# Optimization experiments

Hardware: AMD Instinct MI355X
Metric: run time of the kernel (lower is better)

Reference implementation:

```python
import jax, jax.numpy as jnp
import numpy as np

B, N, M = 256, 2207, 16          # graphs per batch, nodes per graph, mid_channel
E = 16777216                      # total edges in the batched graph
C1, C2 = 12, 4                    # global_conv1_dim, global_conv2_dim
H1, H2 = 256, 64                  # FC hidden sizes
EPS = 1e-5                        # LayerNorm / BatchNorm eps
BN_SCALE = 1.0 / np.sqrt(1.0 + EPS)  # eval BatchNorm with running_mean=0, running_var=1


def setup_inputs() -> dict:
    ks = jax.random.split(jax.random.key(0), 16)
    def nrm(i, shape, s):
        return jax.random.normal(ks[i], shape, jnp.float32) * s
    return {
        "x": jax.random.normal(ks[0], (B * N, 1), jnp.float32),
        "edge_index": jax.random.randint(ks[1], (2, E), 0, B * N, dtype=jnp.int32),
        "edge_weight": jax.random.uniform(ks[2], (E,), jnp.float32),
        # GraphConv: lin_rel (with bias) on aggregated neighbors + lin_root on self
        "w_root": nrm(3, (1, M), 0.5),
        "w_rel": nrm(4, (1, M), 0.5),
        "b_rel": jnp.full((M,), 0.01, jnp.float32),
        # LayerNorm over (num_nodes, mid_channel)
        "ln_g": jnp.ones((N, M), jnp.float32),
        "ln_b": jnp.zeros((N, M), jnp.float32),
        # 1x1 conv stacks
        "gc1_w": nrm(5, (C1, M), 0.3), "gc1_b": nrm(6, (C1,), 0.1),
        "bn1_g": jnp.ones((C1,), jnp.float32), "bn1_b": jnp.zeros((C1,), jnp.float32),
        "gc2_w": nrm(7, (C2, C1), 0.3), "gc2_b": nrm(8, (C2,), 0.1),
        "bn2_g": jnp.ones((C2,), jnp.float32), "bn2_b": jnp.zeros((C2,), jnp.float32),
        # FC stack (weights stored [in, out])
        "fc_w1": nrm(9, (C2 * N, H1), 0.02), "fc_b1": jnp.full((H1,), 0.01, jnp.float32),
        "fbn1_g": jnp.ones((H1,), jnp.float32), "fbn1_b": jnp.zeros((H1,), jnp.float32),
        "fc_w2": nrm(10, (H1, H2), 0.1), "fc_b2": jnp.full((H2,), 0.01, jnp.float32),
        "fbn2_g": jnp.ones((H2,), jnp.float32), "fbn2_b": jnp.zeros((H2,), jnp.float32),
        "fc1_w": nrm(11, (H2, 1), 0.1), "fc1_b": jnp.full((1,), 0.01, jnp.float32),
    }


def reference(x, edge_index, edge_weight, w_root, w_rel, b_rel, ln_g, ln_b,
              gc1_w, gc1_b, bn1_g, bn1_b, gc2_w, gc2_b, bn2_g, bn2_b,
              fc_w1, fc_b1, fbn1_g, fbn1_b, fc_w2, fc_b2, fbn2_g, fbn2_b,
              fc1_w, fc1_b):
    src, dst = edge_index[0], edge_index[1]
    # GraphConv: gather source features, weight, scatter-add to destinations
    agg = jax.ops.segment_sum(x[src] * edge_weight[:, None], dst, num_segments=B * N)
    h = jax.nn.relu(agg @ w_rel + b_rel + x @ w_root)          # [B*N, M]
    h = h.reshape(B, N, M)
    # LayerNorm over (N, M) per sample (biased variance, as in torch)
    mu = h.mean(axis=(1, 2), keepdims=True)
    var = ((h - mu) ** 2).mean(axis=(1, 2), keepdims=True)
    h = (h - mu) * jax.lax.rsqrt(var + EPS) * ln_g + ln_b
    h = h.transpose(0, 2, 1)                                   # [B, M, N]
    # 1x1 conv -> relu -> eval-BN (rm=0, rv=1)
    y = jax.nn.relu(jnp.einsum('oc,bcn->bon', gc1_w, h) + gc1_b[None, :, None])
    y = y * (BN_SCALE * bn1_g)[None, :, None] + bn1_b[None, :, None]
    y = jax.nn.relu(jnp.einsum('oc,bcn->bon', gc2_w, y) + gc2_b[None, :, None])
    y = y * (BN_SCALE * bn2_g)[None, :, None] + bn2_b[None, :, None]
    z = y.reshape(B, C2 * N)                                   # channel-major flatten, matches torch view
    z = z @ fc_w1 + fc_b1
    z = jax.nn.relu(z * (BN_SCALE * fbn1_g) + fbn1_b)
    z = z @ fc_w2 + fc_b2
    z = jax.nn.relu(z * (BN_SCALE * fbn2_g) + fbn2_b)
    return z @ fc1_w + fc1_b                                   # [B, 1]
```

## Files before the change

### kernel.cpp

```cpp
#include <hip/hip_runtime.h>
#include <hip/hip_bf16.h>

#define BB   256
#define NN   2207
#define MM   16
#define EE   16777216
#define CC1  12
#define CC2  4
#define HH1  256
#define HH2  64
#define KK1  (CC2*NN)
#define LN_EPS 1e-5f
#define BN_SCALE 0.9999950000374997f
#define NBK  256
#define MAGIC 1946067ull
#define EPB  4096
#define TPB  512
#define EPT  (EPB/TPB)
#define NBLK (EE/EPB)

static __device__ __forceinline__ unsigned bucket_of(int d) {
    return (unsigned)(((unsigned long long)(unsigned)d * MAGIC) >> 32);
}

__global__ __launch_bounds__(TPB, 8)
void k_place4(const int* __restrict__ src, const int* __restrict__ dst,
              const float* __restrict__ ew,
              uint2* __restrict__ recs, unsigned short* __restrict__ stab)
{
    __shared__ unsigned int hist[NBK], start[NBK];
    __shared__ unsigned int wtot[4];

    const int t = threadIdx.x;
    if (t < NBK) hist[t] = 0;
    __syncthreads();

    const int i4base = blockIdx.x * (EPB/4);
    unsigned key[EPT];
    float    wv[EPT];
    unsigned short rk[EPT];
    unsigned char  bk[EPT];
    #pragma unroll
    for (int q = 0; q < EPT/4; ++q) {
        int i4 = i4base + q*TPB + t;
        int4   s4 = reinterpret_cast<const int4*>(src)[i4];
        int4   d4 = reinterpret_cast<const int4*>(dst)[i4];
        float4 w4 = reinterpret_cast<const float4*>(ew)[i4];
        unsigned b0 = bucket_of(d4.x), b1 = bucket_of(d4.y);
        unsigned b2 = bucket_of(d4.z), b3 = bucket_of(d4.w);
        unsigned r0 = atomicAdd(&hist[b0], 1u);
        unsigned r1 = atomicAdd(&hist[b1], 1u);
        unsigned r2 = atomicAdd(&hist[b2], 1u);
        unsigned r3 = atomicAdd(&hist[b3], 1u);
        key[q*4+0] = ((unsigned)s4.x << 12) | (unsigned)(d4.x - (int)(b0*NN));
        key[q*4+1] = ((unsigned)s4.y << 12) | (unsigned)(d4.y - (int)(b1*NN));
        key[q*4+2] = ((unsigned)s4.z << 12) | (unsigned)(d4.z - (int)(b2*NN));
        key[q*4+3] = ((unsigned)s4.w << 12) | (unsigned)(d4.w - (int)(b3*NN));
        wv[q*4+0] = w4.x; wv[q*4+1] = w4.y; wv[q*4+2] = w4.z; wv[q*4+3] = w4.w;
        rk[q*4+0] = (unsigned short)r0; rk[q*4+1] = (unsigned short)r1;
        rk[q*4+2] = (unsigned short)r2; rk[q*4+3] = (unsigned short)r3;
        bk[q*4+0] = (unsigned char)b0; bk[q*4+1] = (unsigned char)b1;
        bk[q*4+2] = (unsigned char)b2; bk[q*4+3] = (unsigned char)b3;
    }
    __syncthreads();

    if (t < NBK) {
        unsigned h = hist[t], v = h;
        #pragma unroll
        for (int off = 1; off < 64; off <<= 1) {
            unsigned u = __shfl_up(v, off);
            if ((t & 63) >= off) v += u;
        }
        start[t] = v - h;
        if ((t & 63) == 63) wtot[t >> 6] = v;
    }
    __syncthreads();
    if (t < NBK) {
        const int w = t >> 6;
        unsigned wo = 0;
        if (w > 0) wo += wtot[0];
        if (w > 1) wo += wtot[1];
        if (w > 2) wo += wtot[2];
        start[t] += wo;
        stab[blockIdx.x * NBK + t] = (unsigned short)(start[t]);
    }
    __syncthreads();

    uint2* rb = recs + (size_t)blockIdx.x * EPB;
    #pragma unroll
    for (int e = 0; e < EPT; ++e)
        rb[start[bk[e]] + (unsigned)rk[e]] =
            make_uint2(key[e], __float_as_uint(wv[e]));
}

#define RTPB 256
__global__ __launch_bounds__(RTPB, 8)
void k_replay3(const uint2* __restrict__ recs, const unsigned short* __restrict__ stab,
               const float* __restrict__ x, float* __restrict__ paggr, int rspl)
{
    __shared__ float acc[NN];
    const int t = threadIdx.x;
    const int j = blockIdx.x & (NBK - 1);
    const int r = blockIdx.x >> 8;
    const int kpr = NBLK / rspl;
    for (int n = t; n < NN; n += RTPB) acc[n] = 0.f;
    __syncthreads();

    const int gid = t >> 4, l16 = t & 15;
    const int kb0 = r * kpr;
    for (int kb_i = gid; kb_i < kpr; kb_i += RTPB/16) {
        const int kb = kb0 + kb_i;
        unsigned s0 = stab[(size_t)kb * NBK + j];
        unsigned s1 = (j < NBK-1) ? (unsigned)stab[(size_t)kb * NBK + j + 1]
                                  : (unsigned)EPB;
        const uint2* rp = recs + (size_t)kb * EPB;
        for (unsigned u = s0 + (unsigned)l16; u < s1; u += 16u) {
            uint2 rec = rp[u];
            atomicAdd(&acc[rec.x & 0xFFFu],
                      x[rec.x >> 12] * __uint_as_float(rec.y));
        }
    }
    __syncthreads();
    float* pa = paggr + ((size_t)r * NBK + j) * NN;
    for (int n = t; n < NN; n += RTPB) pa[n] = acc[n];
}

__global__ __launch_bounds__(512)
void k_ln_conv(const float* __restrict__ x, const float* __restrict__ paggr,
              const float* __restrict__ w_root, const float* __restrict__ w_rel,
              const float* __restrict__ b_rel,
              const float* __restrict__ ln_g, const float* __restrict__ ln_b,
              const float* __restrict__ gc1_w, const float* __restrict__ gc1_b,
              const float* __restrict__ bn1_g, const float* __restrict__ bn1_b,
              const float* __restrict__ gc2_w, const float* __restrict__ gc2_b,
              const float* __restrict__ bn2_g, const float* __restrict__ bn2_b,
              float* __restrict__ z, int rspl)
{
    __shared__ float xs[NN], acc[NN];
    __shared__ float gw1[CC1*MM], gb1[CC1], sb1[CC1], tb1[CC1];
    __shared__ float gw2[CC2*CC1], gb2[CC2], sb2[CC2], tb2[CC2];
    __shared__ float redS[8], redQ[8];
    __shared__ float s_mu, s_rs;

    const int b = blockIdx.x, t = threadIdx.x;
    const float* xb = x + b*NN;
    for (int n = t; n < NN; n += 512) {
        xs[n] = xb[n];
        float a = 0.f;
        for (int r = 0; r < rspl; ++r)
            a += paggr[((size_t)r * NBK + b) * NN + n];
        acc[n] = a;
    }
    if (t < CC1*MM) gw1[t] = gc1_w[t];
    if (t >= 192 && t < 192+CC1) { int o = t-192; gb1[o]=gc1_b[o]; sb1[o]=BN_SCALE*bn1_g[o]; tb1[o]=bn1_b[o]; }
    if (t >= 208 && t < 208+CC2*CC1) gw2[t-208] = gc2_w[t-208];
    if (t >= 240 && t < 240+CC2) { int p=t-240; gb2[p]=gc2_b[p]; sb2[p]=BN_SCALE*bn2_g[p]; tb2[p]=bn2_b[p]; }

    float wr[MM], br[MM], wo[MM];
    #pragma unroll
    for (int m = 0; m < MM; ++m) { wr[m]=w_rel[m]; br[m]=b_rel[m]; wo[m]=w_root[m]; }
    __syncthreads();

    float S = 0.f, Q = 0.f;
    for (int n = t; n < NN; n += 512) {
        float a = acc[n], xv = xs[n];
        #pragma unroll
        for (int m = 0; m < MM; ++m) {
            float h = fmaxf(fmaf(a, wr[m], fmaf(xv, wo[m], br[m])), 0.f);
            S += h; Q += h*h;
        }
    }
    #pragma unroll
    for (int off = 32; off; off >>= 1) { S += __shfl_down(S, off); Q += __shfl_down(Q, off); }
    if ((t & 63) == 0) { redS[t>>6] = S; redQ[t>>6] = Q; }
    __syncthreads();
    if (t == 0) {
        float SS = 0.f, QQ = 0.f;
        #pragma unroll
        for (int i = 0; i < 8; ++i) { SS += redS[i]; QQ += redQ[i]; }
        const float inv = 1.f / (float)(NN*MM);
        float mu = SS * inv;
        float var = QQ * inv - mu*mu;
        s_mu = mu; s_rs = rsqrtf(var + LN_EPS);
    }
    __syncthreads();
    const float mu = s_mu, rs = s_rs;

    float* zb = z + (size_t)b * KK1;
    for (int n = t; n < NN; n += 512) {
        float a = acc[n], xv = xs[n];
        float hn[MM];
        const float4* g4  = reinterpret_cast<const float4*>(ln_g + n*MM);
        const float4* be4 = reinterpret_cast<const float4*>(ln_b + n*MM);
        #pragma unroll
        for (int q = 0; q < 4; ++q) {
            float4 g = g4[q], be = be4[q];
            float gg[4]  = {g.x, g.y, g.z, g.w};
            float bb_[4] = {be.x, be.y, be.z, be.w};
            #pragma unroll
            for (int j = 0; j < 4; ++j) {
                int m = q*4 + j;
                float h = fmaxf(fmaf(a, wr[m], fmaf(xv, wo[m], br[m])), 0.f);
                hn[m] = (h - mu) * rs * gg[j] + bb_[j];
            }
        }
        float y1[CC1];
        #pragma unroll
        for (int o = 0; o < CC1; ++o) {
            float a1 = gb1[o];
            #pragma unroll
            for (int m = 0; m < MM; ++m) a1 = fmaf(gw1[o*MM+m], hn[m], a1);
            y1[o] = fmaxf(a1, 0.f) * sb1[o] + tb1[o];
        }
        #pragma unroll
        for (int p = 0; p < CC2; ++p) {
            float a2 = gb2[p];
            #pragma unroll
            for (int o = 0; o < CC1; ++o) a2 = fmaf(gw2[p*CC1+o], y1[o], a2);
            zb[p*NN + n] = fmaxf(a2, 0.f) * sb2[p] + tb2[p];
        }
    }
}

#define GK_CHUNK 288
__global__ __launch_bounds__(256)
void k_fc1_part(const float* __restrict__ z, const float* __restrict__ W1,
                float* __restrict__ out1_part)
{
    __shared__ float zs[64*36];
    __shared__ float ws_[32*68];
    const int bt = blockIdx.x, jt = blockIdx.y, ks = blockIdx.z;
    const int t = threadIdx.x;
    const int tb = t >> 4, tj = t & 15;
    const int k0 = ks * GK_CHUNK;
    const int kend = min(k0 + GK_CHUNK, KK1);
    float acc[4][4] = {};
    const int zrow = t >> 2, zcol = (t & 3) * 8;
    const int wrow = t >> 3, wcol = (t & 7) * 8;

    for (int kc = k0; kc < kend; kc += 32) {
        const float* zsrc = z + (size_t)(bt*64 + zrow)*KK1 + kc + zcol;
        #pragma unroll
        for (int q = 0; q < 2; ++q) {
            int k = kc + zcol + q*4;
            float4 v;
            if (k + 3 < kend) v = *reinterpret_cast<const float4*>(zsrc + q*4);
            else {
                v.x = (k+0 < kend) ? zsrc[q*4+0] : 0.f;
                v.y = (k+1 < kend) ? zsrc[q*4+1] : 0.f;
                v.z = (k+2 < kend) ? zsrc[q*4+2] : 0.f;
                v.w = (k+3 < kend) ? zsrc[q*4+3] : 0.f;
            }
            *reinterpret_cast<float4*>(&zs[zrow*36 + zcol + q*4]) = v;
        }
        {
            int k = kc + wrow;
            const float* wsrc = W1 + (size_t)k*HH1 + jt*64 + wcol;
            #pragma unroll
            for (int q = 0; q < 2; ++q) {
                float4 v;
                if (k < kend) v = *reinterpret_cast<const float4*>(wsrc + q*4);
                else v = float4{0.f,0.f,0.f,0.f};
                *reinterpret_cast<float4*>(&ws_[wrow*68 + wcol + q*4]) = v;
            }
        }
        __syncthreads();
        #pragma unroll
        for (int kk = 0; kk < 32; ++kk) {
            float4 w4 = *reinterpret_cast<const float4*>(&ws_[kk*68 + tj*4]);
            float zv[4], wv[4] = {w4.x, w4.y, w4.z, w4.w};
            #pragma unroll
            for (int ib = 0; ib < 4; ++ib) zv[ib] = zs[(tb*4+ib)*36 + kk];
            #pragma unroll
            for (int ib = 0; ib < 4; ++ib)
                #pragma unroll
                for (int ij = 0; ij < 4; ++ij)
                    acc[ib][ij] = fmaf(zv[ib], wv[ij], acc[ib][ij]);
        }
        __syncthreads();
    }
    #pragma unroll
    for (int ib = 0; ib < 4; ++ib) {
        int row = bt*64 + tb*4 + ib;
        float4 v = make_float4(acc[ib][0], acc[ib][1], acc[ib][2], acc[ib][3]);
        *reinterpret_cast<float4*>(
            &out1_part[((size_t)ks*256 + row)*HH1 + jt*64 + tj*4]) = v;
    }
}

__global__ __launch_bounds__(256)
void k_tail_part(const float* __restrict__ out1_part,
            const float* __restrict__ fc_b1, const float* __restrict__ fbn1_g,
            const float* __restrict__ fbn1_b,
            const float* __restrict__ W2, const float* __restrict__ fc_b2,
            const float* __restrict__ fbn2_g, const float* __restrict__ fbn2_b,
            const float* __restrict__ fc1_w, const float* __restrict__ fc1_b,
            float* __restrict__ out)
{
    __shared__ float o1s[HH1];
    const int b = blockIdx.x, t = threadIdx.x;
    float raw = fc_b1[t];
    #pragma unroll 4
    for (int ks = 0; ks < 31; ++ks)
        raw += out1_part[((size_t)ks*256 + b)*HH1 + t];
    o1s[t] = fmaxf(raw * (BN_SCALE * fbn1_g[t]) + fbn1_b[t], 0.f);
    __syncthreads();
    if (t < HH2) {
        float acc = fc_b2[t];
        #pragma unroll 4
        for (int j = 0; j < HH1; ++j) acc = fmaf(o1s[j], W2[j*HH2 + t], acc);
        float v2 = fmaxf(acc * (BN_SCALE * fbn2_g[t]) + fbn2_b[t], 0.f);
        float c = v2 * fc1_w[t];
        #pragma unroll
        for (int off = 32; off; off >>= 1) c += __shfl_down(c, off);
        if (t == 0) out[b] = c + fc1_b[0];
    }
}

__global__ __launch_bounds__(256)
void k_edge(const int* __restrict__ src, const int* __restrict__ dst,
            const float* __restrict__ ew, const float* __restrict__ x,
            float* __restrict__ agg)
{
    int i = blockIdx.x * 256 + threadIdx.x;
    const int4   s4 = reinterpret_cast<const int4*>(src)[i];
    const int4   d4 = reinterpret_cast<const int4*>(dst)[i];
    const float4 w4 = reinterpret_cast<const float4*>(ew)[i];
    unsafeAtomicAdd(&agg[d4.x], x[s4.x] * w4.x);
    unsafeAtomicAdd(&agg[d4.y], x[s4.y] * w4.y);
    unsafeAtomicAdd(&agg[d4.z], x[s4.z] * w4.z);
    unsafeAtomicAdd(&agg[d4.w], x[s4.w] * w4.w);
}

__global__ __launch_bounds__(256)
void k_sample(const float* __restrict__ x, const float* __restrict__ agg,
              const float* __restrict__ w_root, const float* __restrict__ w_rel,
              const float* __restrict__ b_rel,
              const float* __restrict__ ln_g, const float* __restrict__ ln_b,
              const float* __restrict__ gc1_w, const float* __restrict__ gc1_b,
              const float* __restrict__ bn1_g, const float* __restrict__ bn1_b,
              const float* __restrict__ gc2_w, const float* __restrict__ gc2_b,
              const float* __restrict__ bn2_g, const float* __restrict__ bn2_b,
              float* __restrict__ z)
{
    __shared__ float xs[NN], as[NN];
    __shared__ float gw1[CC1*MM], gb1[CC1], sb1[CC1], tb1[CC1];
    __shared__ float gw2[CC2*CC1], gb2[CC2], sb2[CC2], tb2[CC2];
    __shared__ float redS[4], redQ[4];
    __shared__ float s_mu, s_rs;

    const int b = blockIdx.x, t = threadIdx.x;
    const float* xb = x + b*NN;
    const float* ab = agg + b*NN;
    for (int n = t; n < NN; n += 256) { xs[n] = xb[n]; as[n] = ab[n]; }
    if (t < CC1*MM) gw1[t] = gc1_w[t];
    if (t >= 192 && t < 192+CC1) { int o = t-192; gb1[o]=gc1_b[o]; sb1[o]=BN_SCALE*bn1_g[o]; tb1[o]=bn1_b[o]; }
    if (t >= 208 && t < 208+CC2*CC1) gw2[t-208] = gc2_w[t-208];
    if (t >= 240 && t < 240+CC2) { int p=t-240; gb2[p]=gc2_b[p]; sb2[p]=BN_SCALE*bn2_g[p]; tb2[p]=bn2_b[p]; }

    float wr[MM], br[MM], wo[MM];
    #pragma unroll
    for (int m = 0; m < MM; ++m) { wr[m]=w_rel[m]; br[m]=b_rel[m]; wo[m]=w_root[m]; }
    __syncthreads();

    float S = 0.f, Q = 0.f;
    for (int n = t; n < NN; n += 256) {
        float a = as[n], xv = xs[n];
        #pragma unroll
        for (int m = 0; m < MM; ++m) {
            float h = fmaxf(fmaf(a, wr[m], fmaf(xv, wo[m], br[m])), 0.f);
            S += h; Q += h*h;
        }
    }
    #pragma unroll
    for (int off = 32; off; off >>= 1) { S += __shfl_down(S, off); Q += __shfl_down(Q, off); }
    if ((t & 63) == 0) { redS[t>>6] = S; redQ[t>>6] = Q; }
    __syncthreads();
    if (t == 0) {
        float SS = redS[0]+redS[1]+redS[2]+redS[3];
        float QQ = redQ[0]+redQ[1]+redQ[2]+redQ[3];
        const float inv = 1.f / (float)(NN*MM);
        float mu = SS * inv;
        float var = QQ * inv - mu*mu;
        s_mu = mu; s_rs = rsqrtf(var + LN_EPS);
    }
    __syncthreads();
    const float mu = s_mu, rs = s_rs;

    float* zb = z + (size_t)b * KK1;
    for (int n = t; n < NN; n += 256) {
        float a = as[n], xv = xs[n];
        float hn[MM];
        const float4* g4  = reinterpret_cast<const float4*>(ln_g + n*MM);
        const float4* be4 = reinterpret_cast<const float4*>(ln_b + n*MM);
        #pragma unroll
        for (int q = 0; q < 4; ++q) {
            float4 g = g4[q], be = be4[q];
            float gg[4]  = {g.x, g.y, g.z, g.w};
            float bb_[4] = {be.x, be.y, be.z, be.w};
            #pragma unroll
            for (int j = 0; j < 4; ++j) {
                int m = q*4 + j;
                float h = fmaxf(fmaf(a, wr[m], fmaf(xv, wo[m], br[m])), 0.f);
                hn[m] = (h - mu) * rs * gg[j] + bb_[j];
            }
        }
        float y1[CC1];
        #pragma unroll
        for (int o = 0; o < CC1; ++o) {
            float a1 = gb1[o];
            #pragma unroll
            for (int m = 0; m < MM; ++m) a1 = fmaf(gw1[o*MM+m], hn[m], a1);
            y1[o] = fmaxf(a1, 0.f) * sb1[o] + tb1[o];
        }
        #pragma unroll
        for (int p = 0; p < CC2; ++p) {
            float a2 = gb2[p];
            #pragma unroll
            for (int o = 0; o < CC1; ++o) a2 = fmaf(gw2[p*CC1+o], y1[o], a2);
            zb[p*NN + n] = fmaxf(a2, 0.f) * sb2[p] + tb2[p];
        }
    }
}

__global__ __launch_bounds__(256)
void k_fc1(const float* __restrict__ z, const float* __restrict__ W1,
           float* __restrict__ out1_raw)
{
    __shared__ float zs[64*36];
    __shared__ float ws_[32*68];
    const int bt = blockIdx.x, jt = blockIdx.y, ks = blockIdx.z;
    const int t = threadIdx.x;
    const int tb = t >> 4, tj = t & 15;
    const int k0 = ks * GK_CHUNK;
    const int kend = min(k0 + GK_CHUNK, KK1);
    float acc[4][4] = {};
    const int zrow = t >> 2, zcol = (t & 3) * 8;
    const int wrow = t >> 3, wcol = (t & 7) * 8;

    for (int kc = k0; kc < kend; kc += 32) {
        const float* zsrc = z + (size_t)(bt*64 + zrow)*KK1 + kc + zcol;
        #pragma unroll
        for (int q = 0; q < 2; ++q) {
            int k = kc + zcol + q*4;
            float4 v;
            if (k + 3 < kend) v = *reinterpret_cast<const float4*>(zsrc + q*4);
            else {
                v.x = (k+0 < kend) ? zsrc[q*4+0] : 0.f;
                v.y = (k+1 < kend) ? zsrc[q*4+1] : 0.f;
                v.z = (k+2 < kend) ? zsrc[q*4+2] : 0.f;
                v.w = (k+3 < kend) ? zsrc[q*4+3] : 0.f;
            }
            *reinterpret_cast<float4*>(&zs[zrow*36 + zcol + q*4]) = v;
        }
        {
            int k = kc + wrow;
            const float* wsrc = W1 + (size_t)k*HH1 + jt*64 + wcol;
            #pragma unroll
            for (int q = 0; q < 2; ++q) {
                float4 v;
                if (k < kend) v = *reinterpret_cast<const float4*>(wsrc + q*4);
                else v = float4{0.f,0.f,0.f,0.f};
                *reinterpret_cast<float4*>(&ws_[wrow*68 + wcol + q*4]) = v;
            }
        }
        __syncthreads();
        #pragma unroll
        for (int kk = 0; kk < 32; ++kk) {
            float4 w4 = *reinterpret_cast<const float4*>(&ws_[kk*68 + tj*4]);
            float zv[4], wv[4] = {w4.x, w4.y, w4.z, w4.w};
            #pragma unroll
            for (int ib = 0; ib < 4; ++ib) zv[ib] = zs[(tb*4+ib)*36 + kk];
            #pragma unroll
            for (int ib = 0; ib < 4; ++ib)
                #pragma unroll
                for (int ij = 0; ij < 4; ++ij)
                    acc[ib][ij] = fmaf(zv[ib], wv[ij], acc[ib][ij]);
        }
        __syncthreads();
    }
    #pragma unroll
    for (int ib = 0; ib < 4; ++ib) {
        int row = bt*64 + tb*4 + ib;
        #pragma unroll
        for (int ij = 0; ij < 4; ++ij)
            unsafeAtomicAdd(&out1_raw[row*HH1 + jt*64 + tj*4 + ij], acc[ib][ij]);
    }
}

__global__ __launch_bounds__(256)
void k_tail(const float* __restrict__ out1_raw,
            const float* __restrict__ fc_b1, const float* __restrict__ fbn1_g,
            const float* __restrict__ fbn1_b,
            const float* __restrict__ W2, const float* __restrict__ fc_b2,
            const float* __restrict__ fbn2_g, const float* __restrict__ fbn2_b,
            const float* __restrict__ fc1_w, const float* __restrict__ fc1_b,
            float* __restrict__ out)
{
    __shared__ float o1s[HH1];
    const int b = blockIdx.x, t = threadIdx.x;
    float raw = out1_raw[b*HH1 + t] + fc_b1[t];
    o1s[t] = fmaxf(raw * (BN_SCALE * fbn1_g[t]) + fbn1_b[t], 0.f);
    __syncthreads();
    if (t < HH2) {
        float acc = fc_b2[t];
        #pragma unroll 4
        for (int j = 0; j < HH1; ++j) acc = fmaf(o1s[j], W2[j*HH2 + t], acc);
        float v2 = fmaxf(acc * (BN_SCALE * fbn2_g[t]) + fbn2_b[t], 0.f);
        float c = v2 * fc1_w[t];
        #pragma unroll
        for (int off = 32; off; off >>= 1) c += __shfl_down(c, off);
        if (t == 0) out[b] = c + fc1_b[0];
    }
}

extern "C" void kernel_launch(void* const* d_in, const int* in_sizes, int n_in,
                              void* d_out, int out_size, void* d_ws, size_t ws_size,
                              hipStream_t stream)
{
    const float* x      = (const float*)d_in[0];
    const int*   ei     = (const int*)  d_in[1];
    const float* ew     = (const float*)d_in[2];
    const float* w_root = (const float*)d_in[3];
    const float* w_rel  = (const float*)d_in[4];
    const float* b_rel  = (const float*)d_in[5];
    const float* ln_g   = (const float*)d_in[6];
    const float* ln_b   = (const float*)d_in[7];
    const float* gc1_w  = (const float*)d_in[8];
    const float* gc1_b  = (const float*)d_in[9];
    const float* bn1_g  = (const float*)d_in[10];
    const float* bn1_b  = (const float*)d_in[11];
    const float* gc2_w  = (const float*)d_in[12];
    const float* gc2_b  = (const float*)d_in[13];
    const float* bn2_g  = (const float*)d_in[14];
    const float* bn2_b  = (const float*)d_in[15];
    const float* fc_w1  = (const float*)d_in[16];
    const float* fc_b1  = (const float*)d_in[17];
    const float* fbn1_g = (const float*)d_in[18];
    const float* fbn1_b = (const float*)d_in[19];
    const float* fc_w2  = (const float*)d_in[20];
    const float* fc_b2  = (const float*)d_in[21];
    const float* fbn2_g = (const float*)d_in[22];
    const float* fbn2_b = (const float*)d_in[23];
    const float* fc1_w  = (const float*)d_in[24];
    const float* fc1_b  = (const float*)d_in[25];
    float* out = (float*)d_out;

    char* ws = (char*)d_ws;
    const size_t off_recs  = 0;
    const size_t off_stab  = off_recs + (size_t)NBLK*EPB*8;
    const size_t off_paggr = off_stab + (size_t)NBLK*NBK*2;
    const size_t o1p_sz    = (size_t)31*HH1*256*4;

    int rspl = 8;
    size_t pg_sz   = (size_t)rspl*NBK*NN*4;
    if (pg_sz < o1p_sz) pg_sz = o1p_sz;
    size_t off_zbuf = off_paggr + pg_sz;
    size_t need     = off_zbuf + (size_t)BB*KK1*4;
    if (ws_size < need) {
        rspl = 4;
        pg_sz = (size_t)rspl*NBK*NN*4;
        off_zbuf = off_paggr + pg_sz;
        need = off_zbuf + (size_t)BB*KK1*4;
    }

    if (ws_size >= need) {
        uint2*          recs  = (uint2*)(ws + off_recs);
        unsigned short* stab  = (unsigned short*)(ws + off_stab);
        float*          paggr = (float*)(ws + off_paggr);
        float*          zbuf  = (float*)(ws + off_zbuf);
        float*          o1p   = (float*)(ws + off_paggr);

        k_place4<<<NBLK, TPB, 0, stream>>>(ei, ei + EE, ew, recs, stab);
        k_replay3<<<NBK*rspl, RTPB, 0, stream>>>(recs, stab, x, paggr, rspl);
        k_ln_conv<<<BB, 512, 0, stream>>>(x, paggr,
                                         w_root, w_rel, b_rel, ln_g, ln_b,
                                         gc1_w, gc1_b, bn1_g, bn1_b,
                                         gc2_w, gc2_b, bn2_g, bn2_b, zbuf, rspl);
        k_fc1_part<<<dim3(4,4,31), 256, 0, stream>>>(zbuf, fc_w1, o1p);
        k_tail_part<<<BB, 256, 0, stream>>>(o1p, fc_b1, fbn1_g, fbn1_b,
                                       fc_w2, fc_b2, fbn2_g, fbn2_b,
                                       fc1_w, fc1_b, out);
    } else {
        float* agg      = (float*)(ws);
        float* zbuf     = (float*)(ws + 2259968);
        float* out1_raw = (float*)(ws + 2259968 + 9039872);

        hipMemsetAsync(agg,      0, (size_t)BB*NN*sizeof(float),  stream);
        hipMemsetAsync(out1_raw, 0, (size_t)BB*HH1*sizeof(float), stream);

        k_edge<<<EE/4/256, 256, 0, stream>>>(ei, ei + EE, ew, x, agg);
        k_sample<<<BB, 256, 0, stream>>>(x, agg, w_root, w_rel, b_rel, ln_g, ln_b,
                                         gc1_w, gc1_b, bn1_g, bn1_b,
                                         gc2_w, gc2_b, bn2_g, bn2_b, zbuf);
        k_fc1<<<dim3(4,4,31), 256, 0, stream>>>(zbuf, fc_w1, out1_raw);
        k_tail<<<BB, 256, 0, stream>>>(out1_raw, fc_b1, fbn1_g, fbn1_b,
                                       fc_w2, fc_b2, fbn2_g, fbn2_b,
                                       fc1_w, fc1_b, out);
    }
}
```

Measured before the change: 314.5 us.

## Replace per-block bucket records with global counting sort into contiguous per-graph segments

Edge bucketing becomes a full counting sort: a count pass builds per-block bucket histograms, a scan computes global per-bucket bases, and the placement pass writes each graph's edges into one contiguous padded segment. The replay kernel then streams that segment with 16-byte loads, split into a fixed number of slices, instead of walking thousands of small per-block ranges through a stab table. This is meant to remove the short, uneven inner loops and the stab lookups in replay. The price is an extra full read of dst plus two small scan launches, and the scratch layout is fixed at four slices.

```diff
diff --git a/kernel.cpp b/kernel.cpp
--- a/kernel.cpp
+++ b/kernel.cpp
@@ -18,21 +18,95 @@
 #define TPB  512
 #define EPT  (EPB/TPB)
 #define NBLK (EE/EPB)
+#define RSPL 4
 
 static __device__ __forceinline__ unsigned bucket_of(int d) {
     return (unsigned)(((unsigned long long)(unsigned)d * MAGIC) >> 32);
 }
 
-__global__ __launch_bounds__(TPB, 8)
-void k_place4(const int* __restrict__ src, const int* __restrict__ dst,
-              const float* __restrict__ ew,
-              uint2* __restrict__ recs, unsigned short* __restrict__ stab)
-{
-    __shared__ unsigned int hist[NBK], start[NBK];
-    __shared__ unsigned int wtot[4];
-
+__global__ __launch_bounds__(TPB)
+void k_cnt(const int* __restrict__ dst, unsigned int* __restrict__ cnt)
+{
+    __shared__ unsigned int hist[NBK];
     const int t = threadIdx.x;
     if (t < NBK) hist[t] = 0;
+    __syncthreads();
+    const int i4base = blockIdx.x * (EPB/4);
+    #pragma unroll
+    for (int q = 0; q < EPT/4; ++q) {
+        int4 d4 = reinterpret_cast<const int4*>(dst)[i4base + q*TPB + t];
+        atomicAdd(&hist[bucket_of(d4.x)], 1u);
+        atomicAdd(&hist[bucket_of(d4.y)], 1u);
+        atomicAdd(&hist[bucket_of(d4.z)], 1u);
+        atomicAdd(&hist[bucket_of(d4.w)], 1u);
+    }
+    __syncthreads();
+    if (t < NBK) cnt[blockIdx.x * NBK + t] = hist[t];
+}
+
+__global__ __launch_bounds__(256)
+void k_scan(const unsigned int* __restrict__ cnt,
+            unsigned int* __restrict__ base, unsigned int* __restrict__ lens)
+{
+    __shared__ unsigned int wsum[4];
+    const int j = blockIdx.x, t = threadIdx.x, w = t >> 6;
+    unsigned run = 0;
+    for (int c = 0; c < NBLK/256; ++c) {
+        int blk = c*256 + t;
+        unsigned v = cnt[blk * NBK + j];
+        unsigned s = v;
+        #pragma unroll
+        for (int off = 1; off < 64; off <<= 1) {
+            unsigned u = __shfl_up(s, off);
+            if ((t & 63) >= off) s += u;
+        }
+        if ((t & 63) == 63) wsum[w] = s;
+        __syncthreads();
+        unsigned wo = 0, tot = 0;
+        #pragma unroll
+        for (int k = 0; k < 4; ++k) { unsigned x = wsum[k]; tot += x; if (k < w) wo += x; }
+        base[blk * NBK + j] = run + wo + (s - v);
+        run += tot;
+        __syncthreads();
+    }
+    if (t == 0) lens[j] = run;
+}
+
+__global__ __launch_bounds__(256)
+void k_off(const unsigned int* __restrict__ lens, unsigned int* __restrict__ off,
+           uint2* __restrict__ pairs)
+{
+    __shared__ unsigned int wsum[4];
+    const int t = threadIdx.x, w = t >> 6;
+    unsigned len = lens[t];
+    unsigned pl = (len + 3u) & ~3u;
+    unsigned s = pl;
+    #pragma unroll
+    for (int o = 1; o < 64; o <<= 1) {
+        unsigned u = __shfl_up(s, o);
+        if ((t & 63) >= o) s += u;
+    }
+    if ((t & 63) == 63) wsum[w] = s;
+    __syncthreads();
+    unsigned wo = 0;
+    #pragma unroll
+    for (int k = 0; k < 4; ++k) if (k < w) wo += wsum[k];
+    unsigned o0 = wo + s - pl;
+    off[t] = o0;
+    if (t == 255) off[256] = o0 + pl;
+    for (unsigned g = len; g < pl; ++g) pairs[o0 + g] = make_uint2(0u, 0u);
+}
+
+__global__ __launch_bounds__(TPB, 8)
+void k_place_d(const int* __restrict__ src, const int* __restrict__ dst,
+               const float* __restrict__ ew,
+               const unsigned int* __restrict__ base,
+               const unsigned int* __restrict__ off,
+               uint2* __restrict__ pairs)
+{
+    __shared__ unsigned int hist[NBK], babs[NBK];
+    const int t = threadIdx.x;
+    if (t < NBK) { hist[t] = 0; babs[t] = off[t] + base[blockIdx.x * NBK + t]; }
     __syncthreads();
 
     const int i4base = blockIdx.x * (EPB/4);
@@ -62,67 +136,38 @@
         bk[q*4+0] = (unsigned char)b0; bk[q*4+1] = (unsigned char)b1;
         bk[q*4+2] = (unsigned char)b2; bk[q*4+3] = (unsigned char)b3;
     }
-    __syncthreads();
-
-    if (t < NBK) {
-        unsigned h = hist[t], v = h;
-        #pragma unroll
-        for (int off = 1; off < 64; off <<= 1) {
-            unsigned u = __shfl_up(v, off);
-            if ((t & 63) >= off) v += u;
-        }
-        start[t] = v - h;
-        if ((t & 63) == 63) wtot[t >> 6] = v;
-    }
-    __syncthreads();
-    if (t < NBK) {
-        const int w = t >> 6;
-        unsigned wo = 0;
-        if (w > 0) wo += wtot[0];
-        if (w > 1) wo += wtot[1];
-        if (w > 2) wo += wtot[2];
-        start[t] += wo;
-        stab[blockIdx.x * NBK + t] = (unsigned short)(start[t]);
-    }
-    __syncthreads();
-
-    uint2* rb = recs + (size_t)blockIdx.x * EPB;
     #pragma unroll
     for (int e = 0; e < EPT; ++e)
-        rb[start[bk[e]] + (unsigned)rk[e]] =
+        pairs[(size_t)babs[bk[e]] + (unsigned)rk[e]] =
             make_uint2(key[e], __float_as_uint(wv[e]));
 }
 
-#define RTPB 256
-__global__ __launch_bounds__(RTPB, 8)
-void k_replay3(const uint2* __restrict__ recs, const unsigned short* __restrict__ stab,
-               const float* __restrict__ x, float* __restrict__ paggr, int rspl)
+#define RCB 512
+__global__ __launch_bounds__(RCB, 8)
+void k_replay_c(const uint2* __restrict__ pairs, const unsigned int* __restrict__ off,
+                const float* __restrict__ x, float* __restrict__ paggr)
 {
     __shared__ float acc[NN];
     const int t = threadIdx.x;
     const int j = blockIdx.x & (NBK - 1);
     const int r = blockIdx.x >> 8;
-    const int kpr = NBLK / rspl;
-    for (int n = t; n < NN; n += RTPB) acc[n] = 0.f;
-    __syncthreads();
-
-    const int gid = t >> 4, l16 = t & 15;
-    const int kb0 = r * kpr;
-    for (int kb_i = gid; kb_i < kpr; kb_i += RTPB/16) {
-        const int kb = kb0 + kb_i;
-        unsigned s0 = stab[(size_t)kb * NBK + j];
-        unsigned s1 = (j < NBK-1) ? (unsigned)stab[(size_t)kb * NBK + j + 1]
-                                  : (unsigned)EPB;
-        const uint2* rp = recs + (size_t)kb * EPB;
-        for (unsigned u = s0 + (unsigned)l16; u < s1; u += 16u) {
-            uint2 rec = rp[u];
-            atomicAdd(&acc[rec.x & 0xFFFu],
-                      x[rec.x >> 12] * __uint_as_float(rec.y));
-        }
+    for (int n = t; n < NN; n += RCB) acc[n] = 0.f;
+    __syncthreads();
+
+    const unsigned o0 = off[j], o1 = off[j + 1];
+    const uint4* p4 = reinterpret_cast<const uint4*>(pairs + o0);
+    const unsigned n4 = (o1 - o0) >> 1;
+    const unsigned q = (n4 + RSPL - 1) / RSPL;
+    const unsigned lo = (unsigned)r * q;
+    const unsigned hi = min(lo + q, n4);
+    for (unsigned e = lo + (unsigned)t; e < hi; e += RCB) {
+        uint4 a = p4[e];
+        atomicAdd(&acc[a.x & 0xFFFu], x[a.x >> 12] * __uint_as_float(a.y));
+        atomicAdd(&acc[a.z & 0xFFFu], x[a.z >> 12] * __uint_as_float(a.w));
     }
     __syncthreads();
     float* pa = paggr + ((size_t)r * NBK + j) * NN;
-    for (int n = t; n < NN; n += RTPB) pa[n] = acc[n];
+    for (int n = t; n < NN; n += RCB) pa[n] = acc[n];
 }
 
 __global__ __launch_bounds__(512)
@@ -134,7 +179,7 @@
               const float* __restrict__ bn1_g, const float* __restrict__ bn1_b,
               const float* __restrict__ gc2_w, const float* __restrict__ gc2_b,
               const float* __restrict__ bn2_g, const float* __restrict__ bn2_b,
-              float* __restrict__ z, int rspl)
+              float* __restrict__ z)
 {
     __shared__ float xs[NN], acc[NN];
     __shared__ float gw1[CC1*MM], gb1[CC1], sb1[CC1], tb1[CC1];
@@ -147,7 +192,8 @@
     for (int n = t; n < NN; n += 512) {
         xs[n] = xb[n];
         float a = 0.f;
-        for (int r = 0; r < rspl; ++r)
+        #pragma unroll
+        for (int r = 0; r < RSPL; ++r)
             a += paggr[((size_t)r * NBK + b) * NN + n];
         acc[n] = a;
     }
@@ -547,36 +593,36 @@
     float* out = (float*)d_out;
 
     char* ws = (char*)d_ws;
-    const size_t off_recs  = 0;
-    const size_t off_stab  = off_recs + (size_t)NBLK*EPB*8;
-    const size_t off_paggr = off_stab + (size_t)NBLK*NBK*2;
-    const size_t o1p_sz    = (size_t)31*HH1*256*4;
-
-    int rspl = 8;
-    size_t pg_sz   = (size_t)rspl*NBK*NN*4;
-    if (pg_sz < o1p_sz) pg_sz = o1p_sz;
-    size_t off_zbuf = off_paggr + pg_sz;
-    size_t need     = off_zbuf + (size_t)BB*KK1*4;
-    if (ws_size < need) {
-        rspl = 4;
-        pg_sz = (size_t)rspl*NBK*NN*4;
-        off_zbuf = off_paggr + pg_sz;
-        need = off_zbuf + (size_t)BB*KK1*4;
-    }
+    const size_t off_pairs = 0;
+    const size_t sz_pairs  = (size_t)(EE + 1024) * 8;
+    const size_t off_offs  = off_pairs + sz_pairs;
+    const size_t off_R     = off_offs + 4096;
+    const size_t sz_R      = (size_t)RSPL*NBK*NN*4;
+    const size_t off_cnt   = off_R;
+    const size_t off_base  = off_R + (size_t)NBLK*NBK*4;
+    const size_t off_lens  = off_R + 2*(size_t)NBLK*NBK*4;
+    const size_t off_zbuf  = off_R + sz_R;
+    const size_t need      = off_zbuf + (size_t)BB*KK1*4;
 
     if (ws_size >= need) {
-        uint2*          recs  = (uint2*)(ws + off_recs);
-        unsigned short* stab  = (unsigned short*)(ws + off_stab);
-        float*          paggr = (float*)(ws + off_paggr);
-        float*          zbuf  = (float*)(ws + off_zbuf);
-        float*          o1p   = (float*)(ws + off_paggr);
-
-        k_place4<<<NBLK, TPB, 0, stream>>>(ei, ei + EE, ew, recs, stab);
-        k_replay3<<<NBK*rspl, RTPB, 0, stream>>>(recs, stab, x, paggr, rspl);
+        uint2*        pairs = (uint2*)(ws + off_pairs);
+        unsigned int* offs  = (unsigned int*)(ws + off_offs);
+        unsigned int* cnt   = (unsigned int*)(ws + off_cnt);
+        unsigned int* base  = (unsigned int*)(ws + off_base);
+        unsigned int* lens  = (unsigned int*)(ws + off_lens);
+        float*        paggr = (float*)(ws + off_R);
+        float*        zbuf  = (float*)(ws + off_zbuf);
+        float*        o1p   = (float*)(ws + off_R);
+
+        k_cnt<<<NBLK, TPB, 0, stream>>>(ei + EE, cnt);
+        k_scan<<<NBK, 256, 0, stream>>>(cnt, base, lens);
+        k_off<<<1, 256, 0, stream>>>(lens, offs, pairs);
+        k_place_d<<<NBLK, TPB, 0, stream>>>(ei, ei + EE, ew, base, offs, pairs);
+        k_replay_c<<<NBK*RSPL, RCB, 0, stream>>>(pairs, offs, x, paggr);
         k_ln_conv<<<BB, 512, 0, stream>>>(x, paggr,
                                          w_root, w_rel, b_rel, ln_g, ln_b,
                                          gc1_w, gc1_b, bn1_g, bn1_b,
-                                         gc2_w, gc2_b, bn2_g, bn2_b, zbuf, rspl);
+                                         gc2_w, gc2_b, bn2_g, bn2_b, zbuf);
         k_fc1_part<<<dim3(4,4,31), 256, 0, stream>>>(zbuf, fc_w1, o1p);
         k_tail_part<<<BB, 256, 0, stream>>>(o1p, fc_b1, fbn1_g, fbn1_b,
                                        fc_w2, fc_b2, fbn2_g, fbn2_b,
```

New measurement: 350.6 us. 1.11x slower.

## Replay four buckets per wavefront with prefetched offsets and more region splits

Applied to the files above, without the earlier changes.

The edge-replay kernel now gives each block a group of four adjacent destination buckets, each held in its own LDS accumulator. A full 64-lane wavefront walks the contiguous record span of all four buckets at once, instead of 16 lanes per single bucket. The bucket offsets for the next region are prefetched while the current one is processed, and the work is split into 16 region chunks rather than 8. The aim is better lane utilisation and fewer dependent offset loads, at the cost of twice as many partial aggregates written and summed in the LayerNorm kernel, and more LDS per block.

```diff
diff --git a/kernel.cpp b/kernel.cpp
--- a/kernel.cpp
+++ b/kernel.cpp
@@ -18,6 +18,9 @@
 #define TPB  512
 #define EPT  (EPB/TPB)
 #define NBLK (EE/EPB)
+#define GRP  4
+#define NGRP (NBK/GRP)
+#define RSP6 16
 
 static __device__ __forceinline__ unsigned bucket_of(int d) {
     return (unsigned)(((unsigned long long)(unsigned)d * MAGIC) >> 32);
@@ -93,36 +96,47 @@
             make_uint2(key[e], __float_as_uint(wv[e]));
 }
 
-#define RTPB 256
-__global__ __launch_bounds__(RTPB, 8)
-void k_replay3(const uint2* __restrict__ recs, const unsigned short* __restrict__ stab,
-               const float* __restrict__ x, float* __restrict__ paggr, int rspl)
-{
-    __shared__ float acc[NN];
+__global__ __launch_bounds__(512, 8)
+void k_replay6(const uint2* __restrict__ recs, const unsigned short* __restrict__ stab,
+               const float* __restrict__ x, float* __restrict__ paggr)
+{
+    __shared__ float acc[GRP*NN];
     const int t = threadIdx.x;
-    const int j = blockIdx.x & (NBK - 1);
-    const int r = blockIdx.x >> 8;
-    const int kpr = NBLK / rspl;
-    for (int n = t; n < NN; n += RTPB) acc[n] = 0.f;
-    __syncthreads();
-
-    const int gid = t >> 4, l16 = t & 15;
-    const int kb0 = r * kpr;
-    for (int kb_i = gid; kb_i < kpr; kb_i += RTPB/16) {
-        const int kb = kb0 + kb_i;
-        unsigned s0 = stab[(size_t)kb * NBK + j];
-        unsigned s1 = (j < NBK-1) ? (unsigned)stab[(size_t)kb * NBK + j + 1]
-                                  : (unsigned)EPB;
-        const uint2* rp = recs + (size_t)kb * EPB;
-        for (unsigned u = s0 + (unsigned)l16; u < s1; u += 16u) {
+    const int g = blockIdx.x & (NGRP - 1);
+    const int r = blockIdx.x >> 6;
+    for (int n = t; n < GRP*NN; n += 512) acc[n] = 0.f;
+    __syncthreads();
+
+    const int lane = t & 63, w = t >> 6;
+    const int nreg = NBLK / RSP6;
+    const int reg0 = r * nreg;
+    const int j0 = g * GRP;
+
+    int region = reg0 + w;
+    const unsigned short* sb = stab + (size_t)region * NBK + j0;
+    unsigned c0 = sb[0], c1 = sb[1], c2 = sb[2], c3 = sb[3];
+    unsigned c4 = (j0 + GRP < NBK) ? (unsigned)sb[4] : (unsigned)EPB;
+
+    for (int ri = w; ri < nreg; ri += 8) {
+        const unsigned b0 = c0, b1 = c1, b2 = c2, b3 = c3, b4 = c4;
+        const uint2* rp = recs + (size_t)region * EPB;
+        const int regionN = region + 8;
+        if (ri + 8 < nreg) {
+            const unsigned short* sbn = stab + (size_t)regionN * NBK + j0;
+            c0 = sbn[0]; c1 = sbn[1]; c2 = sbn[2]; c3 = sbn[3];
+            c4 = (j0 + GRP < NBK) ? (unsigned)sbn[4] : (unsigned)EPB;
+        }
+        for (unsigned u = b0 + (unsigned)lane; u < b4; u += 64u) {
             uint2 rec = rp[u];
-            atomicAdd(&acc[rec.x & 0xFFFu],
+            unsigned so = (u >= b1) + (u >= b2) + (u >= b3);
+            atomicAdd(&acc[so * NN + (rec.x & 0xFFFu)],
                       x[rec.x >> 12] * __uint_as_float(rec.y));
         }
-    }
-    __syncthreads();
-    float* pa = paggr + ((size_t)r * NBK + j) * NN;
-    for (int n = t; n < NN; n += RTPB) pa[n] = acc[n];
+        region = regionN;
+    }
+    __syncthreads();
+    float* pa = paggr + (((size_t)r * NGRP + g) * GRP) * NN;
+    for (int n = t; n < GRP*NN; n += 512) pa[n] = acc[n];
 }
 
 __global__ __launch_bounds__(512)
@@ -134,7 +148,7 @@
               const float* __restrict__ bn1_g, const float* __restrict__ bn1_b,
               const float* __restrict__ gc2_w, const float* __restrict__ gc2_b,
               const float* __restrict__ bn2_g, const float* __restrict__ bn2_b,
-              float* __restrict__ z, int rspl)
+              float* __restrict__ z)
 {
     __shared__ float xs[NN], acc[NN];
     __shared__ float gw1[CC1*MM], gb1[CC1], sb1[CC1], tb1[CC1];
@@ -144,11 +158,14 @@
 
     const int b = blockIdx.x, t = threadIdx.x;
     const float* xb = x + b*NN;
+    const float* pb = paggr + (((size_t)(b >> 2)) * GRP + (b & 3)) * NN;
+    const size_t rstride = (size_t)NGRP * GRP * NN;
     for (int n = t; n < NN; n += 512) {
         xs[n] = xb[n];
         float a = 0.f;
-        for (int r = 0; r < rspl; ++r)
-            a += paggr[((size_t)r * NBK + b) * NN + n];
+        #pragma unroll
+        for (int r = 0; r < RSP6; ++r)
+            a += pb[(size_t)r * rstride + n];
         acc[n] = a;
     }
     if (t < CC1*MM) gw1[t] = gc1_w[t];
@@ -550,19 +567,9 @@
     const size_t off_recs  = 0;
     const size_t off_stab  = off_recs + (size_t)NBLK*EPB*8;
     const size_t off_paggr = off_stab + (size_t)NBLK*NBK*2;
-    const size_t o1p_sz    = (size_t)31*HH1*256*4;
-
-    int rspl = 8;
-    size_t pg_sz   = (size_t)rspl*NBK*NN*4;
-    if (pg_sz < o1p_sz) pg_sz = o1p_sz;
-    size_t off_zbuf = off_paggr + pg_sz;
-    size_t need     = off_zbuf + (size_t)BB*KK1*4;
-    if (ws_size < need) {
-        rspl = 4;
-        pg_sz = (size_t)rspl*NBK*NN*4;
-        off_zbuf = off_paggr + pg_sz;
-        need = off_zbuf + (size_t)BB*KK1*4;
-    }
+    const size_t sz_paggr  = (size_t)RSP6*NGRP*GRP*NN*4;
+    const size_t off_zbuf  = off_paggr + sz_paggr;
+    const size_t need      = off_zbuf + (size_t)BB*KK1*4;
 
     if (ws_size >= need) {
         uint2*          recs  = (uint2*)(ws + off_recs);
@@ -572,11 +579,11 @@
         float*          o1p   = (float*)(ws + off_paggr);
 
         k_place4<<<NBLK, TPB, 0, stream>>>(ei, ei + EE, ew, recs, stab);
-        k_replay3<<<NBK*rspl, RTPB, 0, stream>>>(recs, stab, x, paggr, rspl);
+        k_replay6<<<NGRP*RSP6, 512, 0, stream>>>(recs, stab, x, paggr);
         k_ln_conv<<<BB, 512, 0, stream>>>(x, paggr,
                                          w_root, w_rel, b_rel, ln_g, ln_b,
                                          gc1_w, gc1_b, bn1_g, bn1_b,
-                                         gc2_w, gc2_b, bn2_g, bn2_b, zbuf, rspl);
+                                         gc2_w, gc2_b, bn2_g, bn2_b, zbuf);
         k_fc1_part<<<dim3(4,4,31), 256, 0, stream>>>(zbuf, fc_w1, o1p);
         k_tail_part<<<BB, 256, 0, stream>>>(o1p, fc_b1, fbn1_g, fbn1_b,
                                        fc_w2, fc_b2, fbn2_g, fbn2_b,
```

Measured after the change: 308.4 us. About the same (-1.9%).
